# Optimization experiments

Measured on AMD Instinct MI355X. Metric: run time of the kernel, lower is better.

## Reference

```python
import jax, jax.numpy as jnp
import numpy as np

BN_EPS = 1e-5
NN_CHUNK = 1024  # unknown points processed per distance-matrix tile


def _batch_ids(cnt, total):
    # contiguous per-batch layout -> batch id of each point via cumsum/searchsorted
    return jnp.searchsorted(jnp.cumsum(cnt), jnp.arange(total), side='right')


def three_nn(unknown, known, ub_id, kb_id):
    """Ragged brute-force 3-NN. Returns (squared dists [N,3], global idx [N,3])."""
    N = unknown.shape[0]
    nchunk = N // NN_CHUNK
    u = unknown.reshape(nchunk, NN_CHUNK, 3)
    ub = ub_id.reshape(nchunk, NN_CHUNK)

    def body(args):
        uc, bc = args
        d2 = jnp.sum((uc[:, None, :] - known[None, :, :]) ** 2, axis=-1)  # [chunk, M]
        d2 = jnp.where(bc[:, None] == kb_id[None, :], d2, jnp.inf)  # mask cross-batch pairs
        neg_d, idx = jax.lax.top_k(-d2, 3)
        return -neg_d, idx

    d2, idx = jax.lax.map(body, (u, ub))
    return d2.reshape(N, 3), idx.reshape(N, 3)


def three_interpolate(known_feats, idx, weight):
    # gather [N,3,C] then inverse-distance weighted sum -> [N,C]
    gathered = known_feats[idx]  # [N,3,C]
    return jnp.einsum('nkc,nk->nc', gathered, weight)


def conv_bn_relu(x, W, gamma, beta):
    # 1x1 Conv2d over [1,C,N,1] == pointwise matmul; BN (training stats) over points
    h = x @ W.T  # [N, C_out]
    mean = jnp.mean(h, axis=0)
    var = jnp.mean((h - mean) ** 2, axis=0)  # biased, as torch BN normalization
    h = (h - mean) * jax.lax.rsqrt(var + BN_EPS) * gamma + beta
    return jax.nn.relu(h)


def setup_inputs() -> dict:
    key = jax.random.key(0)
    ks = jax.random.split(key, 10)
    B, Nper, Mper, C1, C2 = 4, 16384, 4096, 128, 256
    N, M = B * Nper, B * Mper
    unknown = jax.random.normal(ks[0], (N, 3), jnp.float32) * 10.0
    known = jax.random.normal(ks[1], (M, 3), jnp.float32) * 10.0
    unknown_feats = jax.random.normal(ks[2], (N, C1), jnp.float32)
    known_feats = jax.random.normal(ks[3], (M, C2), jnp.float32)
    unknown_batch_cnt = jnp.full((B,), Nper, jnp.int32)
    known_batch_cnt = jnp.full((B,), Mper, jnp.int32)
    Cin = C1 + C2  # 384
    W1 = jax.random.normal(ks[4], (256, Cin), jnp.float32) * (1.0 / np.sqrt(Cin))
    W2 = jax.random.normal(ks[5], (256, 256), jnp.float32) * (1.0 / np.sqrt(256))
    g1 = jnp.ones((256,), jnp.float32); b1 = jnp.zeros((256,), jnp.float32)
    g2 = jnp.ones((256,), jnp.float32); b2 = jnp.zeros((256,), jnp.float32)
    return {"unknown": unknown, "unknown_batch_cnt": unknown_batch_cnt,
            "known": known, "known_batch_cnt": known_batch_cnt,
            "unknown_feats": unknown_feats, "known_feats": known_feats,
            "W1": W1, "g1": g1, "b1": b1, "W2": W2, "g2": g2, "b2": b2}


def reference(unknown, unknown_batch_cnt, known, known_batch_cnt,
              unknown_feats, known_feats, W1, g1, b1, W2, g2, b2):
    ub_id = _batch_ids(unknown_batch_cnt, unknown.shape[0])
    kb_id = _batch_ids(known_batch_cnt, known.shape[0])
    dist, idx = three_nn(unknown, known, ub_id, kb_id)  # squared dists, as CUDA kernel
    dist_recip = 1.0 / (dist + 1e-8)
    weight = dist_recip / jnp.sum(dist_recip, axis=-1, keepdims=True)
    interpolated = three_interpolate(known_feats, idx, weight)  # [N, C2]
    new_features = jnp.concatenate([interpolated, unknown_feats], axis=1)  # [N, C2+C1]
    new_features = conv_bn_relu(new_features, W1, g1, b1)
    new_features = conv_bn_relu(new_features, W2, g2, b2)
    return new_features  # [N, 256]
```

## Files before the change

kernel.cpp:

```cpp
#include <hip/hip_runtime.h>
#include <math.h>

typedef __attribute__((ext_vector_type(8))) short short8;
typedef __attribute__((ext_vector_type(4))) float f32x4;

#define INF 3.0e38f
#define BN_EPS 1e-5f

#define NB 1024
#define XMIN (-64.0f)
#define BW 0.125f
#define INVW 8.0f
#define PA 192

__device__ __forceinline__ unsigned short f2bf(float x) {
    union { float f; unsigned u; } v; v.f = x;
    unsigned r = v.u + 0x7FFF + ((v.u >> 16) & 1);
    return (unsigned short)(r >> 16);
}
__device__ __forceinline__ float bf2f(unsigned short u) {
    return __uint_as_float(((unsigned)u) << 16);
}
__device__ __forceinline__ unsigned long long shflx_u64(unsigned long long v, int m) {
    int lo = __shfl_xor((int)(unsigned)(v & 0xFFFFFFFFULL), m, 64);
    int hi = __shfl_xor((int)(unsigned)(v >> 32), m, 64);
    return ((unsigned long long)(unsigned)hi << 32) | (unsigned)lo;
}

__global__ __launch_bounds__(256) void hist2_kernel(
    const float* __restrict__ kn, const int* __restrict__ kcnt, int M,
    const float* __restrict__ un, const int* __restrict__ ucnt, int N,
    int B, int* __restrict__ kc, int* __restrict__ qc)
{
    int j = blockIdx.x * 256 + threadIdx.x;
    const float* P; const int* C; int* out; int idx;
    if (j < M) { P = kn; C = kcnt; out = kc; idx = j; }
    else { idx = j - M; if (idx >= N) return; P = un; C = ucnt; out = qc; }
    int cum = 0, bb = 0;
    for (int i = 0; i < B; i++) { int c = C[i]; if (idx >= cum) bb = i; cum += c; }
    float x = P[idx * 3];
    int bi = (int)((x - XMIN) * INVW);
    bi = min(max(bi, 0), NB - 1);
    atomicAdd(&out[bb * NB + bi], 1);
}

__global__ __launch_bounds__(1024) void scan2_kernel(
    const int* __restrict__ kc, int* __restrict__ kbs, int* __restrict__ kcur,
    const int* __restrict__ qc, int* __restrict__ qbs, int* __restrict__ qcur,
    int T)
{
    __shared__ int ts[1024];
    const int* cnt = blockIdx.x ? qc : kc;
    int* bs  = blockIdx.x ? qbs : kbs;
    int* cur = blockIdx.x ? qcur : kcur;

    int tid = threadIdx.x;
    int base = tid * 4;
    int v0 = 0, v1 = 0, v2 = 0, v3 = 0;
    if (base + 0 < T) v0 = cnt[base + 0];
    if (base + 1 < T) v1 = cnt[base + 1];
    if (base + 2 < T) v2 = cnt[base + 2];
    if (base + 3 < T) v3 = cnt[base + 3];
    int s = v0 + v1 + v2 + v3;
    ts[tid] = s;
    __syncthreads();
    for (int off = 1; off < 1024; off <<= 1) {
        int t = (tid >= off) ? ts[tid - off] : 0;
        __syncthreads();
        ts[tid] += t;
        __syncthreads();
    }
    int ex = ts[tid] - s;
    if (base + 0 < T) { bs[base + 0] = ex; cur[base + 0] = ex; } ex += v0;
    if (base + 1 < T) { bs[base + 1] = ex; cur[base + 1] = ex; } ex += v1;
    if (base + 2 < T) { bs[base + 2] = ex; cur[base + 2] = ex; } ex += v2;
    if (base + 3 < T) { bs[base + 3] = ex; cur[base + 3] = ex; } ex += v3;
    if (tid == ((T - 1) >> 2)) bs[T] = ts[tid];
}

__global__ __launch_bounds__(256) void scatter2_kernel(
    const float* __restrict__ kn, const int* __restrict__ kcnt, int M,
    const float* __restrict__ un, const int* __restrict__ ucnt, int N,
    int B, int* __restrict__ kcur, float4* __restrict__ kscat,
    int* __restrict__ qcur, float4* __restrict__ qscat)
{
    int j = blockIdx.x * 256 + threadIdx.x;
    const float* P; const int* C; int* cur; float4* out; int idx;
    if (j < M) { P = kn; C = kcnt; cur = kcur; out = kscat; idx = j; }
    else { idx = j - M; if (idx >= N) return; P = un; C = ucnt; cur = qcur; out = qscat; }
    int cum = 0, bb = 0;
    for (int i = 0; i < B; i++) { int c = C[i]; if (idx >= cum) bb = i; cum += c; }
    float x = P[idx * 3], y = P[idx * 3 + 1], z = P[idx * 3 + 2];
    int bi = (int)((x - XMIN) * INVW);
    bi = min(max(bi, 0), NB - 1);
    int pos = atomicAdd(&cur[bb * NB + bi], 1);
    out[pos] = make_float4(x, y, z, __int_as_float(idx));
}

__global__ __launch_bounds__(256) void knn6_kernel(
    const int* __restrict__ ucnt, const int* __restrict__ kbs,
    const float4* __restrict__ qscat, const float4* __restrict__ scat,
    int B, float* __restrict__ wgt, int* __restrict__ idxo)
{
    int tid = threadIdx.x;
    int wv = tid >> 6;
    int lane = tid & 63;
    int qi = lane & 7;
    int r8 = lane >> 3;
    int pbase = blockIdx.x * 32;
    int qpos = pbase + wv * 8 + qi;

    int cum = 0, bb = 0;
    for (int i = 0; i < B; i++) { int c = ucnt[i]; if (pbase >= cum) bb = i; cum += c; }

    float4 qf = qscat[qpos];
    float ux = qf.x, uy = qf.y, uz = qf.z;

    int kst = kbs[bb * NB];
    int ken = kbs[bb * NB + NB];

    int bq = (int)((ux - XMIN) * INVW);
    bq = min(max(bq, 0), NB - 1);
    int sp = kbs[bb * NB + bq];

    int abase = sp - PA / 2;
    if (abase + PA > ken) abase = ken - PA;
    if (abase < kst) abase = kst;
    int aend = min(abase + PA, ken);

    float d0 = INF, d1 = INF, d2v = INF;
    auto upd = [&](float e) {
        float m0 = fmaxf(e, d0), m1 = fmaxf(e, d1);
        d0 = fminf(e, d0); d1 = fminf(m0, d1); d2v = fminf(m1, d2v);
    };
    {
        int alo = abase + r8 * (PA / 8);
        int ahi = min(alo + PA / 8, aend);
        int i = alo;
        for (; i + 4 <= ahi; i += 4) {
            float e[4];
#pragma unroll
            for (int c = 0; c < 4; c++) {
                float4 f = scat[i + c];
                float dx = f.x - ux, dy = f.y - uy, dz = f.z - uz;
                e[c] = __builtin_fmaf(dx, dx, __builtin_fmaf(dy, dy, dz * dz));
            }
#pragma unroll
            for (int c = 0; c < 4; c++) upd(e[c]);
        }
        for (; i < ahi; i++) {
            float4 f = scat[i];
            float dx = f.x - ux, dy = f.y - uy, dz = f.z - uz;
            upd(__builtin_fmaf(dx, dx, __builtin_fmaf(dy, dy, dz * dz)));
        }
    }
#pragma unroll
    for (int s = 8; s <= 32; s <<= 1) {
        float e0 = __shfl_xor(d0, s, 64);
        float e1 = __shfl_xor(d1, s, 64);
        float e2 = __shfl_xor(d2v, s, 64);
        upd(e0); upd(e1); upd(e2);
    }
    float thr = d2v;

    float Wr = fminf(sqrtf(thr), 300.0f);
    int blo = max((int)((ux - Wr - XMIN) * INVW) - 1, 0);
    int bhi = min((int)((ux + Wr - XMIN) * INVW) + 1, NB - 1);
    int pLo = kbs[bb * NB + blo];
    int pHi = kbs[bb * NB + bhi + 1];
    int n = pHi - pLo;
    int eig = (n + 7) >> 3;
    int mylo = pLo + r8 * eig;
    int myhi = min(mylo + eig, pHi);

    unsigned long long k0 = ~0ULL, k1 = ~0ULL, k2 = ~0ULL;
    auto insK = [&](unsigned long long k) {
        bool cc0 = k < k0;
        unsigned long long t0 = cc0 ? k : k0;
        unsigned long long t1 = cc0 ? k0 : k;
        bool cc1 = t1 < k1;
        unsigned long long u0 = cc1 ? t1 : k1;
        unsigned long long u1 = cc1 ? k1 : t1;
        k0 = t0; k1 = u0;
        k2 = u1 < k2 ? u1 : k2;
    };

    int i = mylo;
    for (; i + 8 <= myhi; i += 8) {
        float e[8]; int ix[8];
#pragma unroll
        for (int c = 0; c < 8; c++) {
            float4 f = scat[i + c];
            float dx = f.x - ux, dy = f.y - uy, dz = f.z - uz;
            e[c] = __builtin_fmaf(dx, dx, __builtin_fmaf(dy, dy, dz * dz));
            ix[c] = __float_as_int(f.w);
        }
        float m4a = fminf(fminf(e[0], e[1]), fminf(e[2], e[3]));
        float m4b = fminf(fminf(e[4], e[5]), fminf(e[6], e[7]));
        if (m4a <= thr) {
#pragma unroll
            for (int c = 0; c < 4; c++) {
                if (e[c] <= thr) {
                    insK(((unsigned long long)__float_as_uint(e[c]) << 32) |
                         (unsigned)ix[c]);
                    thr = fminf(thr, __uint_as_float((unsigned)(k2 >> 32)));
                }
            }
        }
        if (m4b <= thr) {
#pragma unroll
            for (int c = 4; c < 8; c++) {
                if (e[c] <= thr) {
                    insK(((unsigned long long)__float_as_uint(e[c]) << 32) |
                         (unsigned)ix[c]);
                    thr = fminf(thr, __uint_as_float((unsigned)(k2 >> 32)));
                }
            }
        }
    }
    for (; i < myhi; i++) {
        float4 f = scat[i];
        float dx = f.x - ux, dy = f.y - uy, dz = f.z - uz;
        float e = __builtin_fmaf(dx, dx, __builtin_fmaf(dy, dy, dz * dz));
        if (e <= thr) {
            insK(((unsigned long long)__float_as_uint(e) << 32) |
                 (unsigned)__float_as_int(f.w));
            thr = fminf(thr, __uint_as_float((unsigned)(k2 >> 32)));
        }
    }

#pragma unroll
    for (int s = 8; s <= 32; s <<= 1) {
        unsigned long long e0 = shflx_u64(k0, s);
        unsigned long long e1 = shflx_u64(k1, s);
        unsigned long long e2 = shflx_u64(k2, s);
        insK(e0); insK(e1); insK(e2);
    }

    if (r8 == 0) {
        float dd0 = __uint_as_float((unsigned)(k0 >> 32));
        float dd1 = __uint_as_float((unsigned)(k1 >> 32));
        float dd2 = __uint_as_float((unsigned)(k2 >> 32));
        float r0 = 1.0f / (dd0 + 1e-8f);
        float r1 = 1.0f / (dd1 + 1e-8f);
        float r2 = 1.0f / (dd2 + 1e-8f);
        float rs = 1.0f / (r0 + r1 + r2);
        int orig = __float_as_int(qf.w);
        wgt[orig * 3 + 0] = r0 * rs;
        wgt[orig * 3 + 1] = r1 * rs;
        wgt[orig * 3 + 2] = r2 * rs;
        idxo[orig * 3 + 0] = (int)(unsigned)k0;
        idxo[orig * 3 + 1] = (int)(unsigned)k1;
        idxo[orig * 3 + 2] = (int)(unsigned)k2;
    }
}

__global__ __launch_bounds__(256) void wconv_kernel(
    const float* __restrict__ W1, const float* __restrict__ W2,
    unsigned short* __restrict__ W1b, unsigned short* __restrict__ W2b,
    int n1, int n2)
{
    int i = blockIdx.x * 256 + threadIdx.x;
    if (i < n1) W1b[i] = f2bf(W1[i]);
    int j = i - n1;
    if (j >= 0 && j < n2) W2b[j] = f2bf(W2[j]);
}

template <int K, int MODE>
__global__ __launch_bounds__(256) void gemm_bf16_kernel(
    const void* __restrict__ Aa, const float* __restrict__ ufeat,
    const unsigned short* __restrict__ W,
    const float* __restrict__ wgt, const int* __restrict__ idxv,
    const float* __restrict__ bnsum, const float* __restrict__ bnsq,
    const float* __restrict__ bng, const float* __restrict__ bnb, float invN,
    void* __restrict__ Cv, float* __restrict__ gsum, float* __restrict__ gsq)
{
    __shared__ unsigned short As[128 * 40];
    __shared__ unsigned short Bs[128 * 40];
    __shared__ float colsum[128];
    __shared__ float colsq[128];
    __shared__ float sc[256], sh[256];

    int tid = threadIdx.x;
    int w = tid >> 6, lane = tid & 63;
    int r = w >> 1, cq = w & 1;
    int m16 = lane & 15, q = lane >> 4;
    int bm = blockIdx.x * 128, bn = blockIdx.y * 128;

    if (MODE == 1) {
        float mean = bnsum[tid] * invN;
        float var = bnsq[tid] * invN - mean * mean;
        float scv = bng[tid] * rsqrtf(var + BN_EPS);
        sc[tid] = scv;
        sh[tid] = bnb[tid] - mean * scv;
    }

    int srow = tid >> 2;
    int kc = (tid & 3) * 8;
    float w0a[2], w1a[2], w2a[2];
    int j0a[2], j1a[2], j2a[2];
    if (MODE == 2) {
#pragma unroll
        for (int t = 0; t < 2; t++) {
            int pp = bm + srow + 64 * t;
            w0a[t] = wgt[pp * 3 + 0]; w1a[t] = wgt[pp * 3 + 1]; w2a[t] = wgt[pp * 3 + 2];
            j0a[t] = idxv[pp * 3 + 0]; j1a[t] = idxv[pp * 3 + 1]; j2a[t] = idxv[pp * 3 + 2];
        }
    }

    f32x4 acc[4][4];
#pragma unroll
    for (int i = 0; i < 4; i++)
#pragma unroll
        for (int j = 0; j < 4; j++) acc[i][j] = (f32x4){0.f, 0.f, 0.f, 0.f};

#pragma unroll
    for (int k0 = 0; k0 < K; k0 += 32) {
        __syncthreads();
#pragma unroll
        for (int t = 0; t < 2; t++) {
            int row = srow + 64 * t;
            int c = k0 + kc;
            ushort4 o0, o1;
            if (MODE == 2) {
                if (c < 256) {
                    const float* f0 = (const float*)Aa + (size_t)j0a[t] * 256 + c;
                    const float* f1 = (const float*)Aa + (size_t)j1a[t] * 256 + c;
                    const float* f2 = (const float*)Aa + (size_t)j2a[t] * 256 + c;
                    float4 x0 = *(const float4*)f0, x1 = *(const float4*)(f0 + 4);
                    float4 y0 = *(const float4*)f1, y1 = *(const float4*)(f1 + 4);
                    float4 z0 = *(const float4*)f2, z1 = *(const float4*)(f2 + 4);
                    float W0 = w0a[t], W1 = w1a[t], W2 = w2a[t];
                    o0.x = f2bf(x0.x * W0 + y0.x * W1 + z0.x * W2);
                    o0.y = f2bf(x0.y * W0 + y0.y * W1 + z0.y * W2);
                    o0.z = f2bf(x0.z * W0 + y0.z * W1 + z0.z * W2);
                    o0.w = f2bf(x0.w * W0 + y0.w * W1 + z0.w * W2);
                    o1.x = f2bf(x1.x * W0 + y1.x * W1 + z1.x * W2);
                    o1.y = f2bf(x1.y * W0 + y1.y * W1 + z1.y * W2);
                    o1.z = f2bf(x1.z * W0 + y1.z * W1 + z1.z * W2);
                    o1.w = f2bf(x1.w * W0 + y1.w * W1 + z1.w * W2);
                } else {
                    const float* fu = ufeat + (size_t)(bm + row) * 128 + (c - 256);
                    float4 u0 = *(const float4*)fu, u1 = *(const float4*)(fu + 4);
                    o0.x = f2bf(u0.x); o0.y = f2bf(u0.y);
                    o0.z = f2bf(u0.z); o0.w = f2bf(u0.w);
                    o1.x = f2bf(u1.x); o1.y = f2bf(u1.y);
                    o1.z = f2bf(u1.z); o1.w = f2bf(u1.w);
                }
            } else {
                const unsigned short* Ab = (const unsigned short*)Aa;
                ushort4 h0 = *(const ushort4*)(Ab + (size_t)(bm + row) * K + c);
                ushort4 h1v = *(const ushort4*)(Ab + (size_t)(bm + row) * K + c + 4);
                float4 s0 = *(const float4*)&sc[c];
                float4 s1 = *(const float4*)&sc[c + 4];
                float4 t0 = *(const float4*)&sh[c];
                float4 t1 = *(const float4*)&sh[c + 4];
                o0.x = f2bf(fmaxf(bf2f(h0.x) * s0.x + t0.x, 0.f));
                o0.y = f2bf(fmaxf(bf2f(h0.y) * s0.y + t0.y, 0.f));
                o0.z = f2bf(fmaxf(bf2f(h0.z) * s0.z + t0.z, 0.f));
                o0.w = f2bf(fmaxf(bf2f(h0.w) * s0.w + t0.w, 0.f));
                o1.x = f2bf(fmaxf(bf2f(h1v.x) * s1.x + t1.x, 0.f));
                o1.y = f2bf(fmaxf(bf2f(h1v.y) * s1.y + t1.y, 0.f));
                o1.z = f2bf(fmaxf(bf2f(h1v.z) * s1.z + t1.z, 0.f));
                o1.w = f2bf(fmaxf(bf2f(h1v.w) * s1.w + t1.w, 0.f));
            }
            *(ushort4*)&As[row * 40 + kc] = o0;
            *(ushort4*)&As[row * 40 + kc + 4] = o1;
            *(short8*)&Bs[row * 40 + kc] =
                *(const short8*)(W + (size_t)(bn + row) * K + k0 + kc);
        }
        __syncthreads();

        short8 af[4], bf[4];
#pragma unroll
        for (int sub = 0; sub < 4; sub++) {
            af[sub] = *(const short8*)&As[(r * 64 + sub * 16 + m16) * 40 + q * 8];
            bf[sub] = *(const short8*)&Bs[(cq * 64 + sub * 16 + m16) * 40 + q * 8];
        }
#pragma unroll
        for (int sm = 0; sm < 4; sm++)
#pragma unroll
            for (int sn = 0; sn < 4; sn++)
                acc[sm][sn] = __builtin_amdgcn_mfma_f32_16x16x32_bf16(
                    af[sm], bf[sn], acc[sm][sn], 0, 0, 0);
    }

    int row0 = bm + r * 64 + q * 4;
    int col0 = bn + cq * 64 + m16;
#pragma unroll
    for (int sm = 0; sm < 4; sm++)
#pragma unroll
        for (int sn = 0; sn < 4; sn++) {
            f32x4 v = acc[sm][sn];
#pragma unroll
            for (int reg = 0; reg < 4; reg++) {
                size_t idx = (size_t)(row0 + sm * 16 + reg) * 256 + col0 + sn * 16;
                if (MODE == 2) ((unsigned short*)Cv)[idx] = f2bf(v[reg]);
                else           ((float*)Cv)[idx] = v[reg];
            }
        }

    __syncthreads();
    if (tid < 128) { colsum[tid] = 0.f; colsq[tid] = 0.f; }
    __syncthreads();
#pragma unroll
    for (int sn = 0; sn < 4; sn++) {
        float sacc = 0.f, qacc = 0.f;
#pragma unroll
        for (int sm = 0; sm < 4; sm++) {
            f32x4 v = acc[sm][sn];
#pragma unroll
            for (int reg = 0; reg < 4; reg++) {
                sacc += v[reg];
                qacc += v[reg] * v[reg];
            }
        }
        int lc = cq * 64 + sn * 16 + m16;
        atomicAdd(&colsum[lc], sacc);
        atomicAdd(&colsq[lc], qacc);
    }
    __syncthreads();
    if (tid < 128) {
        atomicAdd(&gsum[bn + tid], colsum[tid]);
        atomicAdd(&gsq[bn + tid], colsq[tid]);
    }
}

__global__ __launch_bounds__(256) void final_act_kernel(
    const float* __restrict__ h2, const float* __restrict__ bnsum,
    const float* __restrict__ bnsq, const float* __restrict__ bng,
    const float* __restrict__ bnb, float invN,
    float* __restrict__ out, int total4)
{
    __shared__ float sc[256], sh[256];
    int c = threadIdx.x;
    float mean = bnsum[c] * invN;
    float var = bnsq[c] * invN - mean * mean;
    float scv = bng[c] * rsqrtf(var + BN_EPS);
    sc[c] = scv;
    sh[c] = bnb[c] - mean * scv;
    __syncthreads();

    int i = blockIdx.x * 256 + threadIdx.x;
    if (i >= total4) return;
    int c4 = i & 63;
    float4 v = ((const float4*)h2)[i];
    float4 s = *(const float4*)&sc[c4 * 4];
    float4 t = *(const float4*)&sh[c4 * 4];
    float4 o;
    o.x = fmaxf(v.x * s.x + t.x, 0.0f);
    o.y = fmaxf(v.y * s.y + t.y, 0.0f);
    o.z = fmaxf(v.z * s.z + t.z, 0.0f);
    o.w = fmaxf(v.w * s.w + t.w, 0.0f);
    ((float4*)out)[i] = o;
}

extern "C" void kernel_launch(void* const* d_in, const int* in_sizes, int n_in,
                              void* d_out, int out_size, void* d_ws, size_t ws_size,
                              hipStream_t stream)
{
    const float* unknown = (const float*)d_in[0];
    const int*   ucnt    = (const int*)d_in[1];
    const float* known   = (const float*)d_in[2];
    const int*   kcnt    = (const int*)d_in[3];
    const float* ufeat   = (const float*)d_in[4];
    const float* kfeat   = (const float*)d_in[5];
    const float* W1      = (const float*)d_in[6];
    const float* g1      = (const float*)d_in[7];
    const float* b1      = (const float*)d_in[8];
    const float* W2      = (const float*)d_in[9];
    const float* g2      = (const float*)d_in[10];
    const float* b2      = (const float*)d_in[11];

    int N = in_sizes[0] / 3;
    int B = in_sizes[1];
    int M = in_sizes[2] / 3;
    int T = B * NB;

    char* ws = (char*)d_ws;
    size_t off = 0;
    float* wgt = (float*)(ws + off);            off += (size_t)N * 3 * 4;
    int*   idxb = (int*)(ws + off);             off += (size_t)N * 3 * 4;
    float* stats = (float*)(ws + off);          off += 4 * 256 * 4;
    float* sum1 = stats,        *sq1 = stats + 256;
    float* sum2 = stats + 512,  *sq2 = stats + 768;
    int* kch = (int*)(ws + off);                off += (size_t)T * 4;
    int* qch = (int*)(ws + off);                off += (size_t)T * 4;
    int* kbs = (int*)(ws + off);                off += ((size_t)T + 1) * 4;
    int* qbs = (int*)(ws + off);                off += ((size_t)T + 1) * 4;
    int* kcur = (int*)(ws + off);               off += (size_t)T * 4;
    int* qcur = (int*)(ws + off);               off += (size_t)T * 4;
    unsigned short* W1b = (unsigned short*)(ws + off);  off += 256 * 384 * 2;
    unsigned short* W2b = (unsigned short*)(ws + off);  off += 256 * 256 * 2;
    off = (off + 255) & ~(size_t)255;
    float4* kscat = (float4*)(ws + off);        off += (size_t)M * sizeof(float4);
    float4* qscat = (float4*)(ws + off);        off += (size_t)N * sizeof(float4);
    off = (off + 255) & ~(size_t)255;
    unsigned short* h1 = (unsigned short*)(ws + off);   off += (size_t)N * 256 * 2;
    off = (off + 255) & ~(size_t)255;
    float* h2 = (float*)(ws + off);

    float invN = 1.0f / (float)N;

    hipMemsetAsync(stats, 0, 4 * 256 * 4 + 2 * (size_t)T * 4, stream);

    wconv_kernel<<<(256 * 384 + 256 * 256 + 255) / 256, 256, 0, stream>>>(
        W1, W2, W1b, W2b, 256 * 384, 256 * 256);

    hist2_kernel<<<(M + N + 255) / 256, 256, 0, stream>>>(
        known, kcnt, M, unknown, ucnt, N, B, kch, qch);
    scan2_kernel<<<2, 1024, 0, stream>>>(kch, kbs, kcur, qch, qbs, qcur, T);
    scatter2_kernel<<<(M + N + 255) / 256, 256, 0, stream>>>(
        known, kcnt, M, unknown, ucnt, N, B, kcur, kscat, qcur, qscat);
    knn6_kernel<<<N / 32, 256, 0, stream>>>(ucnt, kbs, qscat, kscat,
                                            B, wgt, idxb);

    gemm_bf16_kernel<384, 2><<<dim3(N / 128, 2), 256, 0, stream>>>(
        kfeat, ufeat, W1b, wgt, idxb,
        nullptr, nullptr, nullptr, nullptr, 0.f, h1, sum1, sq1);
    gemm_bf16_kernel<256, 1><<<dim3(N / 128, 2), 256, 0, stream>>>(
        h1, nullptr, W2b, nullptr, nullptr,
        sum1, sq1, g1, b1, invN, h2, sum2, sq2);
    final_act_kernel<<<N / 4, 256, 0, stream>>>(h2, sum2, sq2, g2, b2, invN,
                                                (float*)d_out, N * 64);
}
```

Baseline: 380.2 us.

## Replace 1D x-slab KNN refinement with 2D xy-grid cell search

Adds a second binning of known points into a 64x64 xy grid per batch and sorts queries by 2D cell instead of x-slab. The refinement pass now scans only the grid rows and column ranges that overlap the threshold radius, with the 8 lane groups splitting rows, instead of scanning a whole x-slab. The initial threshold estimate still uses the 1D x-sorted array. This is meant to cut the number of candidate distance evaluations per query. In exchange it adds a third scan, a second scatter of known points, more workspace, and possible load imbalance across rows.

```diff
diff --git a/kernel.cpp b/kernel.cpp
--- a/kernel.cpp
+++ b/kernel.cpp
@@ -9,9 +9,11 @@
 
 #define NB 1024
 #define XMIN (-64.0f)
-#define BW 0.125f
 #define INVW 8.0f
 #define PA 192
+#define NG 64
+#define NG2 4096
+#define GIW 0.5f
 
 __device__ __forceinline__ unsigned short f2bf(float x) {
     union { float f; unsigned u; } v; v.f = x;
@@ -27,41 +29,51 @@
     return ((unsigned long long)(unsigned)hi << 32) | (unsigned)lo;
 }
 
-__global__ __launch_bounds__(256) void hist2_kernel(
+__global__ __launch_bounds__(256) void hist3_kernel(
     const float* __restrict__ kn, const int* __restrict__ kcnt, int M,
     const float* __restrict__ un, const int* __restrict__ ucnt, int N,
-    int B, int* __restrict__ kc, int* __restrict__ qc)
+    int B, int* __restrict__ kc1, int* __restrict__ kc2, int* __restrict__ qc2)
 {
     int j = blockIdx.x * 256 + threadIdx.x;
-    const float* P; const int* C; int* out; int idx;
-    if (j < M) { P = kn; C = kcnt; out = kc; idx = j; }
-    else { idx = j - M; if (idx >= N) return; P = un; C = ucnt; out = qc; }
-    int cum = 0, bb = 0;
-    for (int i = 0; i < B; i++) { int c = C[i]; if (idx >= cum) bb = i; cum += c; }
-    float x = P[idx * 3];
-    int bi = (int)((x - XMIN) * INVW);
-    bi = min(max(bi, 0), NB - 1);
-    atomicAdd(&out[bb * NB + bi], 1);
-}
-
-__global__ __launch_bounds__(1024) void scan2_kernel(
-    const int* __restrict__ kc, int* __restrict__ kbs, int* __restrict__ kcur,
-    const int* __restrict__ qc, int* __restrict__ qbs, int* __restrict__ qcur,
-    int T)
+    if (j < M) {
+        int cum = 0, bb = 0;
+        for (int i = 0; i < B; i++) { int c = kcnt[i]; if (j >= cum) bb = i; cum += c; }
+        float x = kn[j * 3], y = kn[j * 3 + 1];
+        int b1 = min(max((int)((x - XMIN) * INVW), 0), NB - 1);
+        atomicAdd(&kc1[bb * NB + b1], 1);
+        int bx = min(max((int)((x - XMIN) * GIW), 0), NG - 1);
+        int by = min(max((int)((y - XMIN) * GIW), 0), NG - 1);
+        atomicAdd(&kc2[bb * NG2 + by * NG + bx], 1);
+    } else {
+        int idx = j - M; if (idx >= N) return;
+        int cum = 0, bb = 0;
+        for (int i = 0; i < B; i++) { int c = ucnt[i]; if (idx >= cum) bb = i; cum += c; }
+        float x = un[idx * 3], y = un[idx * 3 + 1];
+        int bx = min(max((int)((x - XMIN) * GIW), 0), NG - 1);
+        int by = min(max((int)((y - XMIN) * GIW), 0), NG - 1);
+        atomicAdd(&qc2[bb * NG2 + by * NG + bx], 1);
+    }
+}
+
+__global__ __launch_bounds__(1024) void scan3_kernel(
+    const int* __restrict__ kc1, int* __restrict__ kbs1, int* __restrict__ kcur1,
+    const int* __restrict__ kc2, int* __restrict__ kbs2, int* __restrict__ kcur2,
+    const int* __restrict__ qc2, int* __restrict__ qbs2, int* __restrict__ qcur2,
+    int T1, int T2)
 {
     __shared__ int ts[1024];
-    const int* cnt = blockIdx.x ? qc : kc;
-    int* bs  = blockIdx.x ? qbs : kbs;
-    int* cur = blockIdx.x ? qcur : kcur;
-
+    const int* cnt; int* bs; int* cur; int T;
+    if (blockIdx.x == 0)      { cnt = kc1; bs = kbs1; cur = kcur1; T = T1; }
+    else if (blockIdx.x == 1) { cnt = kc2; bs = kbs2; cur = kcur2; T = T2; }
+    else                      { cnt = qc2; bs = qbs2; cur = qcur2; T = T2; }
     int tid = threadIdx.x;
-    int base = tid * 4;
-    int v0 = 0, v1 = 0, v2 = 0, v3 = 0;
-    if (base + 0 < T) v0 = cnt[base + 0];
-    if (base + 1 < T) v1 = cnt[base + 1];
-    if (base + 2 < T) v2 = cnt[base + 2];
-    if (base + 3 < T) v3 = cnt[base + 3];
-    int s = v0 + v1 + v2 + v3;
+    int v[16]; int s = 0;
+#pragma unroll
+    for (int c = 0; c < 16; c++) {
+        int idx = tid * 16 + c;
+        int val = (idx < T) ? cnt[idx] : 0;
+        v[c] = val; s += val;
+    }
     ts[tid] = s;
     __syncthreads();
     for (int off = 1; off < 1024; off <<= 1) {
@@ -71,35 +83,51 @@
         __syncthreads();
     }
     int ex = ts[tid] - s;
-    if (base + 0 < T) { bs[base + 0] = ex; cur[base + 0] = ex; } ex += v0;
-    if (base + 1 < T) { bs[base + 1] = ex; cur[base + 1] = ex; } ex += v1;
-    if (base + 2 < T) { bs[base + 2] = ex; cur[base + 2] = ex; } ex += v2;
-    if (base + 3 < T) { bs[base + 3] = ex; cur[base + 3] = ex; } ex += v3;
-    if (tid == ((T - 1) >> 2)) bs[T] = ts[tid];
-}
-
-__global__ __launch_bounds__(256) void scatter2_kernel(
+#pragma unroll
+    for (int c = 0; c < 16; c++) {
+        int idx = tid * 16 + c;
+        if (idx < T) { bs[idx] = ex; cur[idx] = ex; }
+        ex += v[c];
+    }
+    if (tid == 1023) bs[T] = ts[1023];
+}
+
+__global__ __launch_bounds__(256) void scatter3_kernel(
     const float* __restrict__ kn, const int* __restrict__ kcnt, int M,
-    const float* __restrict__ un, const int* __restrict__ ucnt, int N,
-    int B, int* __restrict__ kcur, float4* __restrict__ kscat,
-    int* __restrict__ qcur, float4* __restrict__ qscat)
+    const float* __restrict__ un, const int* __restrict__ ucnt, int N, int B,
+    int* __restrict__ kcur1, float4* __restrict__ kscat1,
+    int* __restrict__ kcur2, float4* __restrict__ kscat2,
+    int* __restrict__ qcur2, float4* __restrict__ qscat)
 {
     int j = blockIdx.x * 256 + threadIdx.x;
-    const float* P; const int* C; int* cur; float4* out; int idx;
-    if (j < M) { P = kn; C = kcnt; cur = kcur; out = kscat; idx = j; }
-    else { idx = j - M; if (idx >= N) return; P = un; C = ucnt; cur = qcur; out = qscat; }
-    int cum = 0, bb = 0;
-    for (int i = 0; i < B; i++) { int c = C[i]; if (idx >= cum) bb = i; cum += c; }
-    float x = P[idx * 3], y = P[idx * 3 + 1], z = P[idx * 3 + 2];
-    int bi = (int)((x - XMIN) * INVW);
-    bi = min(max(bi, 0), NB - 1);
-    int pos = atomicAdd(&cur[bb * NB + bi], 1);
-    out[pos] = make_float4(x, y, z, __int_as_float(idx));
-}
-
-__global__ __launch_bounds__(256) void knn6_kernel(
-    const int* __restrict__ ucnt, const int* __restrict__ kbs,
-    const float4* __restrict__ qscat, const float4* __restrict__ scat,
+    if (j < M) {
+        int cum = 0, bb = 0;
+        for (int i = 0; i < B; i++) { int c = kcnt[i]; if (j >= cum) bb = i; cum += c; }
+        float x = kn[j * 3], y = kn[j * 3 + 1], z = kn[j * 3 + 2];
+        float4 f = make_float4(x, y, z, __int_as_float(j));
+        int b1 = min(max((int)((x - XMIN) * INVW), 0), NB - 1);
+        int p1 = atomicAdd(&kcur1[bb * NB + b1], 1);
+        kscat1[p1] = f;
+        int bx = min(max((int)((x - XMIN) * GIW), 0), NG - 1);
+        int by = min(max((int)((y - XMIN) * GIW), 0), NG - 1);
+        int p2 = atomicAdd(&kcur2[bb * NG2 + by * NG + bx], 1);
+        kscat2[p2] = f;
+    } else {
+        int idx = j - M; if (idx >= N) return;
+        int cum = 0, bb = 0;
+        for (int i = 0; i < B; i++) { int c = ucnt[i]; if (idx >= cum) bb = i; cum += c; }
+        float x = un[idx * 3], y = un[idx * 3 + 1], z = un[idx * 3 + 2];
+        int bx = min(max((int)((x - XMIN) * GIW), 0), NG - 1);
+        int by = min(max((int)((y - XMIN) * GIW), 0), NG - 1);
+        int p = atomicAdd(&qcur2[bb * NG2 + by * NG + bx], 1);
+        qscat[p] = make_float4(x, y, z, __int_as_float(idx));
+    }
+}
+
+__global__ __launch_bounds__(256) void knn10_kernel(
+    const int* __restrict__ ucnt, const int* __restrict__ kbs1,
+    const int* __restrict__ kbs2, const float4* __restrict__ qscat,
+    const float4* __restrict__ scat1, const float4* __restrict__ scat2,
     int B, float* __restrict__ wgt, int* __restrict__ idxo)
 {
     int tid = threadIdx.x;
@@ -111,17 +139,16 @@
     int qpos = pbase + wv * 8 + qi;
 
     int cum = 0, bb = 0;
-    for (int i = 0; i < B; i++) { int c = ucnt[i]; if (pbase >= cum) bb = i; cum += c; }
+    for (int i = 0; i < B; i++) { int c = ucnt[i]; if (qpos >= cum) bb = i; cum += c; }
 
     float4 qf = qscat[qpos];
     float ux = qf.x, uy = qf.y, uz = qf.z;
 
-    int kst = kbs[bb * NB];
-    int ken = kbs[bb * NB + NB];
-
-    int bq = (int)((ux - XMIN) * INVW);
-    bq = min(max(bq, 0), NB - 1);
-    int sp = kbs[bb * NB + bq];
+    int kst = kbs1[bb * NB];
+    int ken = kbs1[bb * NB + NB];
+
+    int bq = min(max((int)((ux - XMIN) * INVW), 0), NB - 1);
+    int sp = kbs1[bb * NB + bq];
 
     int abase = sp - PA / 2;
     if (abase + PA > ken) abase = ken - PA;
@@ -141,7 +168,7 @@
             float e[4];
 #pragma unroll
             for (int c = 0; c < 4; c++) {
-                float4 f = scat[i + c];
+                float4 f = scat1[i + c];
                 float dx = f.x - ux, dy = f.y - uy, dz = f.z - uz;
                 e[c] = __builtin_fmaf(dx, dx, __builtin_fmaf(dy, dy, dz * dz));
             }
@@ -149,7 +176,7 @@
             for (int c = 0; c < 4; c++) upd(e[c]);
         }
         for (; i < ahi; i++) {
-            float4 f = scat[i];
+            float4 f = scat1[i];
             float dx = f.x - ux, dy = f.y - uy, dz = f.z - uz;
             upd(__builtin_fmaf(dx, dx, __builtin_fmaf(dy, dy, dz * dz)));
         }
@@ -164,14 +191,10 @@
     float thr = d2v;
 
     float Wr = fminf(sqrtf(thr), 300.0f);
-    int blo = max((int)((ux - Wr - XMIN) * INVW) - 1, 0);
-    int bhi = min((int)((ux + Wr - XMIN) * INVW) + 1, NB - 1);
-    int pLo = kbs[bb * NB + blo];
-    int pHi = kbs[bb * NB + bhi + 1];
-    int n = pHi - pLo;
-    int eig = (n + 7) >> 3;
-    int mylo = pLo + r8 * eig;
-    int myhi = min(mylo + eig, pHi);
+    int bxlo = max((int)((ux - Wr - XMIN) * GIW) - 1, 0);
+    int bxhi = min((int)((ux + Wr - XMIN) * GIW) + 1, NG - 1);
+    int bylo = max((int)((uy - Wr - XMIN) * GIW) - 1, 0);
+    int byhi = min((int)((uy + Wr - XMIN) * GIW) + 1, NG - 1);
 
     unsigned long long k0 = ~0ULL, k1 = ~0ULL, k2 = ~0ULL;
     auto insK = [&](unsigned long long k) {
@@ -185,47 +208,41 @@
         k2 = u1 < k2 ? u1 : k2;
     };
 
-    int i = mylo;
-    for (; i + 8 <= myhi; i += 8) {
-        float e[8]; int ix[8];
-#pragma unroll
-        for (int c = 0; c < 8; c++) {
-            float4 f = scat[i + c];
+    for (int ry = bylo + r8; ry <= byhi; ry += 8) {
+        int rowb = bb * NG2 + ry * NG;
+        int lo = kbs2[rowb + bxlo];
+        int hi = kbs2[rowb + bxhi + 1];
+        int i = lo;
+        for (; i + 4 <= hi; i += 4) {
+            float e[4]; int ix[4];
+#pragma unroll
+            for (int c = 0; c < 4; c++) {
+                float4 f = scat2[i + c];
+                float dx = f.x - ux, dy = f.y - uy, dz = f.z - uz;
+                e[c] = __builtin_fmaf(dx, dx, __builtin_fmaf(dy, dy, dz * dz));
+                ix[c] = __float_as_int(f.w);
+            }
+            float m4 = fminf(fminf(e[0], e[1]), fminf(e[2], e[3]));
+            if (m4 <= thr) {
+#pragma unroll
+                for (int c = 0; c < 4; c++) {
+                    if (e[c] <= thr) {
+                        insK(((unsigned long long)__float_as_uint(e[c]) << 32) |
+                             (unsigned)ix[c]);
+                        thr = fminf(thr, __uint_as_float((unsigned)(k2 >> 32)));
+                    }
+                }
+            }
+        }
+        for (; i < hi; i++) {
+            float4 f = scat2[i];
             float dx = f.x - ux, dy = f.y - uy, dz = f.z - uz;
-            e[c] = __builtin_fmaf(dx, dx, __builtin_fmaf(dy, dy, dz * dz));
-            ix[c] = __float_as_int(f.w);
-        }
-        float m4a = fminf(fminf(e[0], e[1]), fminf(e[2], e[3]));
-        float m4b = fminf(fminf(e[4], e[5]), fminf(e[6], e[7]));
-        if (m4a <= thr) {
-#pragma unroll
-            for (int c = 0; c < 4; c++) {
-                if (e[c] <= thr) {
-                    insK(((unsigned long long)__float_as_uint(e[c]) << 32) |
-                         (unsigned)ix[c]);
-                    thr = fminf(thr, __uint_as_float((unsigned)(k2 >> 32)));
-                }
-            }
-        }
-        if (m4b <= thr) {
-#pragma unroll
-            for (int c = 4; c < 8; c++) {
-                if (e[c] <= thr) {
-                    insK(((unsigned long long)__float_as_uint(e[c]) << 32) |
-                         (unsigned)ix[c]);
-                    thr = fminf(thr, __uint_as_float((unsigned)(k2 >> 32)));
-                }
-            }
-        }
-    }
-    for (; i < myhi; i++) {
-        float4 f = scat[i];
-        float dx = f.x - ux, dy = f.y - uy, dz = f.z - uz;
-        float e = __builtin_fmaf(dx, dx, __builtin_fmaf(dy, dy, dz * dz));
-        if (e <= thr) {
-            insK(((unsigned long long)__float_as_uint(e) << 32) |
-                 (unsigned)__float_as_int(f.w));
-            thr = fminf(thr, __uint_as_float((unsigned)(k2 >> 32)));
+            float e = __builtin_fmaf(dx, dx, __builtin_fmaf(dy, dy, dz * dz));
+            if (e <= thr) {
+                insK(((unsigned long long)__float_as_uint(e) << 32) |
+                     (unsigned)__float_as_int(f.w));
+                thr = fminf(thr, __uint_as_float((unsigned)(k2 >> 32)));
+            }
         }
     }
 
@@ -475,7 +492,8 @@
     int N = in_sizes[0] / 3;
     int B = in_sizes[1];
     int M = in_sizes[2] / 3;
-    int T = B * NB;
+    int T1 = B * NB;
+    int T2 = B * NG2;
 
     char* ws = (char*)d_ws;
     size_t off = 0;
@@ -484,16 +502,20 @@
     float* stats = (float*)(ws + off);          off += 4 * 256 * 4;
     float* sum1 = stats,        *sq1 = stats + 256;
     float* sum2 = stats + 512,  *sq2 = stats + 768;
-    int* kch = (int*)(ws + off);                off += (size_t)T * 4;
-    int* qch = (int*)(ws + off);                off += (size_t)T * 4;
-    int* kbs = (int*)(ws + off);                off += ((size_t)T + 1) * 4;
-    int* qbs = (int*)(ws + off);                off += ((size_t)T + 1) * 4;
-    int* kcur = (int*)(ws + off);               off += (size_t)T * 4;
-    int* qcur = (int*)(ws + off);               off += (size_t)T * 4;
+    int* kc1 = (int*)(ws + off);                off += (size_t)T1 * 4;
+    int* kc2 = (int*)(ws + off);                off += (size_t)T2 * 4;
+    int* qc2 = (int*)(ws + off);                off += (size_t)T2 * 4;
+    int* kbs1 = (int*)(ws + off);               off += ((size_t)T1 + 1) * 4;
+    int* kbs2 = (int*)(ws + off);               off += ((size_t)T2 + 1) * 4;
+    int* qbs2 = (int*)(ws + off);               off += ((size_t)T2 + 1) * 4;
+    int* kcur1 = (int*)(ws + off);              off += (size_t)T1 * 4;
+    int* kcur2 = (int*)(ws + off);              off += (size_t)T2 * 4;
+    int* qcur2 = (int*)(ws + off);              off += (size_t)T2 * 4;
     unsigned short* W1b = (unsigned short*)(ws + off);  off += 256 * 384 * 2;
     unsigned short* W2b = (unsigned short*)(ws + off);  off += 256 * 256 * 2;
     off = (off + 255) & ~(size_t)255;
-    float4* kscat = (float4*)(ws + off);        off += (size_t)M * sizeof(float4);
+    float4* kscat1 = (float4*)(ws + off);       off += (size_t)M * sizeof(float4);
+    float4* kscat2 = (float4*)(ws + off);       off += (size_t)M * sizeof(float4);
     float4* qscat = (float4*)(ws + off);        off += (size_t)N * sizeof(float4);
     off = (off + 255) & ~(size_t)255;
     unsigned short* h1 = (unsigned short*)(ws + off);   off += (size_t)N * 256 * 2;
@@ -502,18 +524,21 @@
 
     float invN = 1.0f / (float)N;
 
-    hipMemsetAsync(stats, 0, 4 * 256 * 4 + 2 * (size_t)T * 4, stream);
+    hipMemsetAsync(stats, 0, 4 * 256 * 4 + ((size_t)T1 + 2 * (size_t)T2) * 4,
+                   stream);
 
     wconv_kernel<<<(256 * 384 + 256 * 256 + 255) / 256, 256, 0, stream>>>(
         W1, W2, W1b, W2b, 256 * 384, 256 * 256);
 
-    hist2_kernel<<<(M + N + 255) / 256, 256, 0, stream>>>(
-        known, kcnt, M, unknown, ucnt, N, B, kch, qch);
-    scan2_kernel<<<2, 1024, 0, stream>>>(kch, kbs, kcur, qch, qbs, qcur, T);
-    scatter2_kernel<<<(M + N + 255) / 256, 256, 0, stream>>>(
-        known, kcnt, M, unknown, ucnt, N, B, kcur, kscat, qcur, qscat);
-    knn6_kernel<<<N / 32, 256, 0, stream>>>(ucnt, kbs, qscat, kscat,
-                                            B, wgt, idxb);
+    hist3_kernel<<<(M + N + 255) / 256, 256, 0, stream>>>(
+        known, kcnt, M, unknown, ucnt, N, B, kc1, kc2, qc2);
+    scan3_kernel<<<3, 1024, 0, stream>>>(kc1, kbs1, kcur1, kc2, kbs2, kcur2,
+                                         qc2, qbs2, qcur2, T1, T2);
+    scatter3_kernel<<<(M + N + 255) / 256, 256, 0, stream>>>(
+        known, kcnt, M, unknown, ucnt, N, B,
+        kcur1, kscat1, kcur2, kscat2, qcur2, qscat);
+    knn10_kernel<<<N / 32, 256, 0, stream>>>(ucnt, kbs1, kbs2, qscat,
+                                             kscat1, kscat2, B, wgt, idxb);
 
     gemm_bf16_kernel<384, 2><<<dim3(N / 128, 2), 256, 0, stream>>>(
         kfeat, ufeat, W1b, wgt, idxb,
```

Measured after the change: 409.2 us. 7.6% more time.
